# Kernel optimization log

Hardware: AMD Instinct MI355X
Metric: run time of the kernel (lower is better)

Reference implementation:

```python
import jax, jax.numpy as jnp
import numpy as np

N, IN, OUT, RANK = 8192, 4096, 4096, 16
SCALING = 2.0

def setup_inputs() -> dict:
    key = jax.random.key(0)
    k1, k2, k3, k4 = jax.random.split(key, 4)
    x = jax.random.normal(k1, (N, IN), dtype=jnp.float32)
    weight = jax.random.normal(k2, (OUT, IN), dtype=jnp.float32) * (1.0 / np.sqrt(IN))
    lora_A = jax.random.normal(k3, (RANK, IN), dtype=jnp.float32) * (1.0 / np.sqrt(IN))
    lora_B = jax.random.normal(k4, (OUT, RANK), dtype=jnp.float32) * 0.01
    return {"x": x, "weight": weight, "lora_A": lora_A, "lora_B": lora_B}

def reference(x, weight, lora_A, lora_B):
    # frozen base linear: F.linear(x, weight) == x @ weight.T  -> [N, OUT]
    base = jnp.einsum('ni,oi->no', x, weight)
    # LoRA branch: dropout(x) (p=0 => identity) @ A.T @ B.T, scaled
    lora = jnp.einsum('ni,ri->nr', x, lora_A)      # [N, RANK]
    lora = jnp.einsum('nr,or->no', lora, lora_B)   # [N, OUT]
    return base + lora * SCALING
```

## Files before the change

### kernel.cpp

```cpp
#include <hip/hip_runtime.h>


#define N_ROWS 8192
#define K_DIM  4096
#define N_COLS 4096
#define RANK   16
#define BK     64
#define NT     (K_DIM / BK)

#define XBLK ((N_ROWS * K_DIM / 4) / 256)
#define WBLK ((N_COLS * K_DIM / 4) / 256)

typedef __bf16 bf16x8 __attribute__((ext_vector_type(8)));
typedef float  f32x4  __attribute__((ext_vector_type(4)));

__device__ __forceinline__ unsigned short f2bf(float f) {
  unsigned int u = __builtin_bit_cast(unsigned int, f);
  u += 0x7FFFu + ((u >> 16) & 1u);
  return (unsigned short)(u >> 16);
}


__global__ __launch_bounds__(256) void prep_kernel(const float* __restrict__ x,
                                                   const float* __restrict__ w,
                                                   const float* __restrict__ A,
                                                   const float* __restrict__ Bm,
                                                   unsigned short* __restrict__ xb,
                                                   unsigned short* __restrict__ wb) {
  const int b = blockIdx.x;
  if (b < XBLK) {
    size_t idx = (size_t)b * 256 + threadIdx.x;
    const float4 v = *reinterpret_cast<const float4*>(x + idx * 4);
    ushort4 r;
    r.x = f2bf(v.x); r.y = f2bf(v.y); r.z = f2bf(v.z); r.w = f2bf(v.w);
    *reinterpret_cast<ushort4*>(xb + idx * 4) = r;
  } else {
    size_t idx = (size_t)(b - XBLK) * 256 + threadIdx.x;
    int o  = (int)(idx >> 10);
    int ic = (int)(idx & 1023) << 2;
    const float4 wv = *reinterpret_cast<const float4*>(w + (size_t)o * K_DIM + ic);
    float a0 = wv.x, a1 = wv.y, a2 = wv.z, a3 = wv.w;
    float br[RANK];
#pragma unroll
    for (int r4 = 0; r4 < RANK / 4; ++r4) {
      const float4 bv = *reinterpret_cast<const float4*>(Bm + (size_t)o * RANK + r4 * 4);
      br[r4 * 4 + 0] = bv.x; br[r4 * 4 + 1] = bv.y;
      br[r4 * 4 + 2] = bv.z; br[r4 * 4 + 3] = bv.w;
    }
#pragma unroll
    for (int r = 0; r < RANK; ++r) {
      const float4 av = *reinterpret_cast<const float4*>(A + (size_t)r * K_DIM + ic);
      float b2 = br[r] * 2.0f;
      a0 += b2 * av.x; a1 += b2 * av.y; a2 += b2 * av.z; a3 += b2 * av.w;
    }
    ushort4 rr;
    rr.x = f2bf(a0); rr.y = f2bf(a1); rr.z = f2bf(a2); rr.w = f2bf(a3);
    *reinterpret_cast<ushort4*>(wb + (size_t)o * K_DIM + ic) = rr;
  }
}


__device__ __forceinline__ void gload_lds16(const void* g, void* l) {
  __builtin_amdgcn_global_load_lds(
      (__attribute__((address_space(1))) void*)g,
      (__attribute__((address_space(3))) void*)l, 16, 0, 0);
}

__global__ __launch_bounds__(512, 1) void gemm_bf16_r7(
    const unsigned short* __restrict__ xb, const unsigned short* __restrict__ wb,
    float* __restrict__ out) {
  __shared__ __align__(16) char smem[131072];

  const int t  = threadIdx.x;
  const int l  = t & 63;
  const int wv = t >> 6;
  const int lr = l & 15;
  const int lk = l >> 4;
  const int wr = wv >> 2;
  const int wc = wv & 3;

  const int bid  = blockIdx.x;
  const int sbid = (bid & 7) * 64 + (bid >> 3);
  const int bm   = sbid >> 4;
  const int bn   = sbid & 15;

  const int srow = t >> 3;
  const int scol = ((t & 7) ^ ((t >> 3) & 7)) << 3;
  const unsigned short* gA = xb + (size_t)(bm * 256 + srow) * K_DIM + scol;
  const unsigned short* gB = wb + (size_t)(bn * 256 + srow) * K_DIM + scol;
  char* ldsA = smem + t * 16;
  char* ldsB = smem + 65536 + t * 16;

#define STG_A(hh, SRC, NB) do {                                                 \
    const unsigned short* _g = (SRC) + (size_t)((hh) * 128) * K_DIM;            \
    char* _l = ldsA + (NB) + (hh) * 16384;                                      \
    gload_lds16(_g, _l);                                                        \
    gload_lds16(_g + (size_t)64 * K_DIM, _l + 8192);                            \
  } while (0)
#define STG_B(hh, SRC, NB) do {                                                 \
    const unsigned short* _g = (SRC) + (size_t)((hh) * 128) * K_DIM;            \
    char* _l = ldsB + (NB) + (hh) * 16384;                                      \
    gload_lds16(_g, _l);                                                        \
    gload_lds16(_g + (size_t)64 * K_DIM, _l + 8192);                            \
  } while (0)

  const int g0   = (lk ^ (lr & 7)) << 4;
  const int g1   = ((lk + 4) ^ (lr & 7)) << 4;
  const int aoff = (wr * 16 + lr) * 128;
  const int boff = (wc * 16 + lr) * 128;

  bf16x8 aF[8];
  bf16x8 bE[4];
  bf16x8 bO[4];
  f32x4 acc[8][4];
#pragma unroll
  for (int m = 0; m < 8; ++m)
#pragma unroll
    for (int n = 0; n < 4; ++n)
      acc[m][n] = (f32x4){0.f, 0.f, 0.f, 0.f};

#define RD_A(BASE) do {                                                         \
    _Pragma("unroll")                                                           \
    for (int m = 0; m < 4; ++m) {                                               \
      aF[2 * m + 0] = *(const bf16x8*)(smem + (BASE) + m * 4096 + aoff + g0);   \
      aF[2 * m + 1] = *(const bf16x8*)(smem + (BASE) + m * 4096 + aoff + g1);   \
    }                                                                           \
  } while (0)
#define RD_B(DST, BASE) do {                                                    \
    _Pragma("unroll")                                                           \
    for (int n = 0; n < 2; ++n) {                                               \
      DST[2 * n + 0] = *(const bf16x8*)(smem + 65536 + (BASE) + n * 8192 + boff + g0); \
      DST[2 * n + 1] = *(const bf16x8*)(smem + 65536 + (BASE) + n * 8192 + boff + g1); \
    }                                                                           \
  } while (0)

#define MFMA_Q(MB, NB0, BF) do {                                                \
    _Pragma("unroll")                                                           \
    for (int mi = 0; mi < 4; ++mi)                                              \
      _Pragma("unroll")                                                         \
      for (int ni = 0; ni < 2; ++ni)                                            \
        _Pragma("unroll")                                                       \
        for (int kk = 0; kk < 2; ++kk)                                          \
          acc[(MB) + mi][(NB0) + ni] = __builtin_amdgcn_mfma_f32_16x16x32_bf16( \
              aF[mi * 2 + kk], BF[ni * 2 + kk], acc[(MB) + mi][(NB0) + ni], 0, 0, 0); \
  } while (0)

#define PRE_LG() do {                                                           \
    __builtin_amdgcn_sched_barrier(0);                                          \
    __builtin_amdgcn_s_barrier();                                               \
    asm volatile("s_waitcnt lgkmcnt(0)");                                       \
    __builtin_amdgcn_sched_barrier(0);                                          \
    __builtin_amdgcn_s_setprio(1);                                              \
  } while (0)
#define PRE_NOLG() do {                                                         \
    __builtin_amdgcn_sched_barrier(0);                                          \
    __builtin_amdgcn_s_barrier();                                               \
    __builtin_amdgcn_sched_barrier(0);                                          \
    __builtin_amdgcn_s_setprio(1);                                              \
  } while (0)
#define POST() do {                                                             \
    __builtin_amdgcn_s_setprio(0);                                              \
    __builtin_amdgcn_sched_barrier(0);                                          \
    __builtin_amdgcn_s_barrier();                                               \
    __builtin_amdgcn_sched_barrier(0);                                          \
  } while (0)
#define POST_VM4() do {                                                         \
    __builtin_amdgcn_s_setprio(0);                                              \
    __builtin_amdgcn_sched_barrier(0);                                          \
    asm volatile("s_waitcnt vmcnt(4)");                                         \
    __builtin_amdgcn_s_barrier();                                               \
    __builtin_amdgcn_sched_barrier(0);                                          \
  } while (0)

#define TILE(CB, NB, T) do {                                                    \
    const int _t1 = ((T) + 1 < NT) ? (T) + 1 : NT - 1;                          \
    const int _t2 = ((T) + 2 < NT) ? (T) + 2 : NT - 1;                          \
    const unsigned short* _sA1 = gA + (size_t)_t1 * BK;                         \
    const unsigned short* _sB1 = gB + (size_t)_t1 * BK;                         \
    const unsigned short* _sA2 = gA + (size_t)_t2 * BK;                         \
    const unsigned short* _sB2 = gB + (size_t)_t2 * BK;                         \
                    \
    STG_A(1, _sA1, NB);                                                         \
    RD_A((CB)); RD_B(bE, (CB));                                                 \
    asm volatile("s_waitcnt lgkmcnt(8)");                                       \
    PRE_LG(); MFMA_Q(0, 0, bE); POST();                                         \
                       \
    STG_B(0, _sB1, NB);                                                         \
    RD_B(bO, (CB) + 16384);                                                     \
    PRE_LG(); MFMA_Q(0, 2, bO); POST();                                         \
                       \
    STG_A(0, _sA2, CB);                                                         \
    RD_A((CB) + 16384);                                                         \
    PRE_LG(); MFMA_Q(4, 2, bO); POST();                                         \
         \
    STG_B(1, _sB2, CB);                                                         \
    PRE_NOLG(); MFMA_Q(4, 0, bE); POST_VM4();                                   \
  } while (0)

  STG_A(0, gA, 0); STG_A(1, gA, 0); STG_B(0, gB, 0); STG_B(1, gB, 0);
  {
    const unsigned short* _pA1 = gA + (size_t)BK;
    const unsigned short* _pB1 = gB + (size_t)BK;
    STG_A(0, _pA1, 32768);
    STG_B(1, _pB1, 32768);
  }
  __builtin_amdgcn_sched_barrier(0);
  asm volatile("s_waitcnt vmcnt(4)");
  __builtin_amdgcn_s_barrier();
  __builtin_amdgcn_sched_barrier(0);

#pragma nounroll
  for (int u = 0; u < NT / 2; ++u) {
    TILE(0, 32768, 2 * u);
    TILE(32768, 0, 2 * u + 1);
  }

  const int orow = bm * 256 + wr * 16 + lk * 4;
  const int ocol = bn * 256 + wc * 16 + lr;
#pragma unroll
  for (int mf = 0; mf < 8; ++mf)
#pragma unroll
    for (int nf = 0; nf < 4; ++nf)
#pragma unroll
      for (int j = 0; j < 4; ++j)
        out[(size_t)(orow + mf * 32 + j) * N_COLS + (ocol + nf * 64)] = acc[mf][nf][j];

#undef STG_A
#undef STG_B
#undef RD_A
#undef RD_B
#undef MFMA_Q
#undef PRE_LG
#undef PRE_NOLG
#undef POST
#undef POST_VM4
#undef TILE
}


__global__ __launch_bounds__(256) void fallback_kernel(const float* __restrict__ x,
                                                       const float* __restrict__ w,
                                                       const float* __restrict__ A,
                                                       const float* __restrict__ Bm,
                                                       float* __restrict__ out) {
  const int o    = blockIdx.x * 256 + threadIdx.x;
  const int nrow = blockIdx.y;
  float bro[RANK];
#pragma unroll
  for (int r = 0; r < RANK; ++r) bro[r] = Bm[(size_t)o * RANK + r] * 2.0f;
  float bacc = 0.f;
  float tacc[RANK];
#pragma unroll
  for (int r = 0; r < RANK; ++r) tacc[r] = 0.f;
  for (int k = 0; k < K_DIM; ++k) {
    float xv = x[(size_t)nrow * K_DIM + k];
    bacc += xv * w[(size_t)o * K_DIM + k];
#pragma unroll
    for (int r = 0; r < RANK; ++r) tacc[r] += xv * A[(size_t)r * K_DIM + k];
  }
  float res = bacc;
#pragma unroll
  for (int r = 0; r < RANK; ++r) res += bro[r] * tacc[r];
  out[(size_t)nrow * N_COLS + o] = res;
}


extern "C" void kernel_launch(void* const* d_in, const int* in_sizes, int n_in,
                              void* d_out, int out_size, void* d_ws, size_t ws_size,
                              hipStream_t stream) {
  const float* x  = (const float*)d_in[0];
  const float* w  = (const float*)d_in[1];
  const float* A  = (const float*)d_in[2];
  const float* Bm = (const float*)d_in[3];
  float* out = (float*)d_out;

  const size_t need = ((size_t)N_ROWS * K_DIM + (size_t)N_COLS * K_DIM) * sizeof(unsigned short);
  if (ws_size < need) {
    dim3 grid(N_COLS / 256, N_ROWS);
    fallback_kernel<<<grid, 256, 0, stream>>>(x, w, A, Bm, out);
    return;
  }

  unsigned short* xb = (unsigned short*)d_ws;
  unsigned short* wb = xb + (size_t)N_ROWS * K_DIM;

  prep_kernel<<<XBLK + WBLK, 256, 0, stream>>>(x, w, A, Bm, xb, wb);

  const int grid_gemm = (N_ROWS / 256) * (N_COLS / 256);
  gemm_bf16_r7<<<grid_gemm, 512, 0, stream>>>(xb, wb, out);
}
```

Baseline: 314.1 us.

## Replace fine-grained interleaved prefetch schedule with simple double-buffered tile loop

Drops the four-phase schedule, which used per-quarter barriers, setprio and a two-tiles-ahead prefetch interleaved with MFMA quarters. Each tile now issues every global->LDS load for the next tile, reads all fragments and runs all MFMAs, then waits for vmcnt(0) and barriers once. This cuts the number of barriers per tile, but global loads only get one tile of compute to hide behind, and the full vmcnt(0) wait can stall. It reads more like a simplification or baseline experiment than a tuned pipeline.

```diff
diff --git a/kernel.cpp b/kernel.cpp
--- a/kernel.cpp
+++ b/kernel.cpp
@@ -66,7 +66,7 @@
       (__attribute__((address_space(3))) void*)l, 16, 0, 0);
 }
 
-__global__ __launch_bounds__(512, 1) void gemm_bf16_r7(
+__global__ __launch_bounds__(512, 1) void gemm_bf16_r8(
     const unsigned short* __restrict__ xb, const unsigned short* __restrict__ wb,
     float* __restrict__ out) {
   __shared__ __align__(16) char smem[131072];
@@ -145,67 +145,34 @@
               aF[mi * 2 + kk], BF[ni * 2 + kk], acc[(MB) + mi][(NB0) + ni], 0, 0, 0); \
   } while (0)
 
-#define PRE_LG() do {                                                           \
+#define TILE(CB, NB, T) do {                                                    \
+    const int _t1 = ((T) + 1 < NT) ? (T) + 1 : NT - 1;                          \
+    const unsigned short* _sA = gA + (size_t)_t1 * BK;                          \
+    const unsigned short* _sB = gB + (size_t)_t1 * BK;                          \
+                                     \
+    STG_A(0, _sA, NB); STG_A(1, _sA, NB);                                       \
+    STG_B(0, _sB, NB); STG_B(1, _sB, NB);                                       \
     __builtin_amdgcn_sched_barrier(0);                                          \
-    __builtin_amdgcn_s_barrier();                                               \
+      \
+    RD_A((CB));                                                                 \
+    RD_B(bE, (CB));                                                             \
+    RD_B(bO, (CB) + 16384);                                                     \
+    MFMA_Q(0, 0, bE);                                                           \
+    MFMA_Q(0, 2, bO);                                                           \
+    RD_A((CB) + 16384);                                                         \
+    MFMA_Q(4, 0, bE);                                                           \
+    MFMA_Q(4, 2, bO);                                                           \
+        \
     asm volatile("s_waitcnt lgkmcnt(0)");                                       \
     __builtin_amdgcn_sched_barrier(0);                                          \
-    __builtin_amdgcn_s_setprio(1);                                              \
-  } while (0)
-#define PRE_NOLG() do {                                                         \
-    __builtin_amdgcn_sched_barrier(0);                                          \
+    asm volatile("s_waitcnt vmcnt(0)");                                         \
     __builtin_amdgcn_s_barrier();                                               \
     __builtin_amdgcn_sched_barrier(0);                                          \
-    __builtin_amdgcn_s_setprio(1);                                              \
-  } while (0)
-#define POST() do {                                                             \
-    __builtin_amdgcn_s_setprio(0);                                              \
-    __builtin_amdgcn_sched_barrier(0);                                          \
-    __builtin_amdgcn_s_barrier();                                               \
-    __builtin_amdgcn_sched_barrier(0);                                          \
-  } while (0)
-#define POST_VM4() do {                                                         \
-    __builtin_amdgcn_s_setprio(0);                                              \
-    __builtin_amdgcn_sched_barrier(0);                                          \
-    asm volatile("s_waitcnt vmcnt(4)");                                         \
-    __builtin_amdgcn_s_barrier();                                               \
-    __builtin_amdgcn_sched_barrier(0);                                          \
-  } while (0)
-
-#define TILE(CB, NB, T) do {                                                    \
-    const int _t1 = ((T) + 1 < NT) ? (T) + 1 : NT - 1;                          \
-    const int _t2 = ((T) + 2 < NT) ? (T) + 2 : NT - 1;                          \
-    const unsigned short* _sA1 = gA + (size_t)_t1 * BK;                         \
-    const unsigned short* _sB1 = gB + (size_t)_t1 * BK;                         \
-    const unsigned short* _sA2 = gA + (size_t)_t2 * BK;                         \
-    const unsigned short* _sB2 = gB + (size_t)_t2 * BK;                         \
-                    \
-    STG_A(1, _sA1, NB);                                                         \
-    RD_A((CB)); RD_B(bE, (CB));                                                 \
-    asm volatile("s_waitcnt lgkmcnt(8)");                                       \
-    PRE_LG(); MFMA_Q(0, 0, bE); POST();                                         \
-                       \
-    STG_B(0, _sB1, NB);                                                         \
-    RD_B(bO, (CB) + 16384);                                                     \
-    PRE_LG(); MFMA_Q(0, 2, bO); POST();                                         \
-                       \
-    STG_A(0, _sA2, CB);                                                         \
-    RD_A((CB) + 16384);                                                         \
-    PRE_LG(); MFMA_Q(4, 2, bO); POST();                                         \
-         \
-    STG_B(1, _sB2, CB);                                                         \
-    PRE_NOLG(); MFMA_Q(4, 0, bE); POST_VM4();                                   \
   } while (0)
 
   STG_A(0, gA, 0); STG_A(1, gA, 0); STG_B(0, gB, 0); STG_B(1, gB, 0);
-  {
-    const unsigned short* _pA1 = gA + (size_t)BK;
-    const unsigned short* _pB1 = gB + (size_t)BK;
-    STG_A(0, _pA1, 32768);
-    STG_B(1, _pB1, 32768);
-  }
   __builtin_amdgcn_sched_barrier(0);
-  asm volatile("s_waitcnt vmcnt(4)");
+  asm volatile("s_waitcnt vmcnt(0)");
   __builtin_amdgcn_s_barrier();
   __builtin_amdgcn_sched_barrier(0);
 
@@ -230,10 +197,6 @@
 #undef RD_A
 #undef RD_B
 #undef MFMA_Q
-#undef PRE_LG
-#undef PRE_NOLG
-#undef POST
-#undef POST_VM4
 #undef TILE
 }
 
@@ -287,5 +250,5 @@
   prep_kernel<<<XBLK + WBLK, 256, 0, stream>>>(x, w, A, Bm, xb, wb);
 
   const int grid_gemm = (N_ROWS / 256) * (N_COLS / 256);
-  gemm_bf16_r7<<<grid_gemm, 512, 0, stream>>>(xb, wb, out);
-}
+  gemm_bf16_r8<<<grid_gemm, 512, 0, stream>>>(xb, wb, out);
+}
```

After: 310.0 us. About the same (-1.3%).

## Switch GEMM inner product to 32x32x16 bf16 MFMA with remapped LDS fragments

Applied to the files above, without the earlier changes.

Replaces the 16x16x32 bf16 MFMA tiling with 32x32x16 MFMA instructions, so each wave computes 4x2 tiles of 32x32 instead of 8x4 tiles of 16x16. LDS fragment reads, the swizzle offsets and the output write-back mapping are reworked to match the new accumulator layout. The aim is fewer MFMA issues and fewer LDS reads per unit of work, since the larger instruction reuses operands more. The output stores now scatter across rows in a different pattern, and the LDS bank-conflict behaviour changes.

```diff
diff --git a/kernel.cpp b/kernel.cpp
--- a/kernel.cpp
+++ b/kernel.cpp
@@ -12,7 +12,7 @@
 #define WBLK ((N_COLS * K_DIM / 4) / 256)
 
 typedef __bf16 bf16x8 __attribute__((ext_vector_type(8)));
-typedef float  f32x4  __attribute__((ext_vector_type(4)));
+typedef float  f32x16 __attribute__((ext_vector_type(16)));
 
 __device__ __forceinline__ unsigned short f2bf(float f) {
   unsigned int u = __builtin_bit_cast(unsigned int, f);
@@ -66,18 +66,18 @@
       (__attribute__((address_space(3))) void*)l, 16, 0, 0);
 }
 
-__global__ __launch_bounds__(512, 1) void gemm_bf16_r7(
+__global__ __launch_bounds__(512, 1) void gemm_bf16_r11(
     const unsigned short* __restrict__ xb, const unsigned short* __restrict__ wb,
     float* __restrict__ out) {
   __shared__ __align__(16) char smem[131072];
 
-  const int t  = threadIdx.x;
-  const int l  = t & 63;
-  const int wv = t >> 6;
-  const int lr = l & 15;
-  const int lk = l >> 4;
-  const int wr = wv >> 2;
-  const int wc = wv & 3;
+  const int t   = threadIdx.x;
+  const int l   = t & 63;
+  const int wv  = t >> 6;
+  const int l31 = l & 31;
+  const int l5  = l >> 5;
+  const int wm  = wv >> 2;
+  const int wn  = wv & 3;
 
   const int bid  = blockIdx.x;
   const int sbid = (bid & 7) * 64 + (bid >> 3);
@@ -104,45 +104,59 @@
     gload_lds16(_g + (size_t)64 * K_DIM, _l + 8192);                            \
   } while (0)
 
-  const int g0   = (lk ^ (lr & 7)) << 4;
-  const int g1   = ((lk + 4) ^ (lr & 7)) << 4;
-  const int aoff = (wr * 16 + lr) * 128;
-  const int boff = (wc * 16 + lr) * 128;
+  const int g0 = ((0 + l5) ^ (l & 7)) << 4;
+  const int g1 = ((2 + l5) ^ (l & 7)) << 4;
+  const int g2 = ((4 + l5) ^ (l & 7)) << 4;
+  const int g3 = ((6 + l5) ^ (l & 7)) << 4;
+  const int base_a = (wm * 32 + l31) * 128;
+  const int base_b = 65536 + (wn * 32 + l31) * 128;
 
   bf16x8 aF[8];
   bf16x8 bE[4];
   bf16x8 bO[4];
-  f32x4 acc[8][4];
-#pragma unroll
-  for (int m = 0; m < 8; ++m)
-#pragma unroll
-    for (int n = 0; n < 4; ++n)
-      acc[m][n] = (f32x4){0.f, 0.f, 0.f, 0.f};
-
-#define RD_A(BASE) do {                                                         \
+  f32x16 acc[4][2];
+#pragma unroll
+  for (int m = 0; m < 4; ++m)
+#pragma unroll
+    for (int n = 0; n < 2; ++n)
+#pragma unroll
+      for (int e = 0; e < 16; ++e)
+        acc[m][n][e] = 0.f;
+
+#define RD_A01(CB_) do {                                                        \
+    aF[0] = *(const bf16x8*)(smem + (CB_) + base_a + g0);                       \
+    aF[1] = *(const bf16x8*)(smem + (CB_) + base_a + g1);                       \
+    aF[2] = *(const bf16x8*)(smem + (CB_) + base_a + g2);                       \
+    aF[3] = *(const bf16x8*)(smem + (CB_) + base_a + g3);                       \
+    aF[4] = *(const bf16x8*)(smem + (CB_) + 8192 + base_a + g0);                \
+    aF[5] = *(const bf16x8*)(smem + (CB_) + 8192 + base_a + g1);                \
+    aF[6] = *(const bf16x8*)(smem + (CB_) + 8192 + base_a + g2);                \
+    aF[7] = *(const bf16x8*)(smem + (CB_) + 8192 + base_a + g3);                \
+  } while (0)
+#define RD_A23(CB_) do {                                                        \
+    aF[0] = *(const bf16x8*)(smem + (CB_) + 16384 + base_a + g0);               \
+    aF[1] = *(const bf16x8*)(smem + (CB_) + 16384 + base_a + g1);               \
+    aF[2] = *(const bf16x8*)(smem + (CB_) + 16384 + base_a + g2);               \
+    aF[3] = *(const bf16x8*)(smem + (CB_) + 16384 + base_a + g3);               \
+    aF[4] = *(const bf16x8*)(smem + (CB_) + 24576 + base_a + g0);               \
+    aF[5] = *(const bf16x8*)(smem + (CB_) + 24576 + base_a + g1);               \
+    aF[6] = *(const bf16x8*)(smem + (CB_) + 24576 + base_a + g2);               \
+    aF[7] = *(const bf16x8*)(smem + (CB_) + 24576 + base_a + g3);               \
+  } while (0)
+#define RD_B(DST, CB_, HOFF) do {                                               \
+    DST[0] = *(const bf16x8*)(smem + (CB_) + (HOFF) + base_b + g0);             \
+    DST[1] = *(const bf16x8*)(smem + (CB_) + (HOFF) + base_b + g1);             \
+    DST[2] = *(const bf16x8*)(smem + (CB_) + (HOFF) + base_b + g2);             \
+    DST[3] = *(const bf16x8*)(smem + (CB_) + (HOFF) + base_b + g3);             \
+  } while (0)
+
+#define MFMA2(M0, NF, BF) do {                                                  \
     _Pragma("unroll")                                                           \
-    for (int m = 0; m < 4; ++m) {                                               \
-      aF[2 * m + 0] = *(const bf16x8*)(smem + (BASE) + m * 4096 + aoff + g0);   \
-      aF[2 * m + 1] = *(const bf16x8*)(smem + (BASE) + m * 4096 + aoff + g1);   \
-    }                                                                           \
-  } while (0)
-#define RD_B(DST, BASE) do {                                                    \
-    _Pragma("unroll")                                                           \
-    for (int n = 0; n < 2; ++n) {                                               \
-      DST[2 * n + 0] = *(const bf16x8*)(smem + 65536 + (BASE) + n * 8192 + boff + g0); \
-      DST[2 * n + 1] = *(const bf16x8*)(smem + 65536 + (BASE) + n * 8192 + boff + g1); \
-    }                                                                           \
-  } while (0)
-
-#define MFMA_Q(MB, NB0, BF) do {                                                \
-    _Pragma("unroll")                                                           \
-    for (int mi = 0; mi < 4; ++mi)                                              \
+    for (int mi = 0; mi < 2; ++mi)                                              \
       _Pragma("unroll")                                                         \
-      for (int ni = 0; ni < 2; ++ni)                                            \
-        _Pragma("unroll")                                                       \
-        for (int kk = 0; kk < 2; ++kk)                                          \
-          acc[(MB) + mi][(NB0) + ni] = __builtin_amdgcn_mfma_f32_16x16x32_bf16( \
-              aF[mi * 2 + kk], BF[ni * 2 + kk], acc[(MB) + mi][(NB0) + ni], 0, 0, 0); \
+      for (int kk = 0; kk < 4; ++kk)                                            \
+        acc[(M0) + mi][(NF)] = __builtin_amdgcn_mfma_f32_32x32x16_bf16(         \
+            aF[mi * 4 + kk], BF[kk], acc[(M0) + mi][(NF)], 0, 0, 0);            \
   } while (0)
 
 #define PRE_LG() do {                                                           \
@@ -179,22 +193,22 @@
     const unsigned short* _sB1 = gB + (size_t)_t1 * BK;                         \
     const unsigned short* _sA2 = gA + (size_t)_t2 * BK;                         \
     const unsigned short* _sB2 = gB + (size_t)_t2 * BK;                         \
-                    \
+               \
     STG_A(1, _sA1, NB);                                                         \
-    RD_A((CB)); RD_B(bE, (CB));                                                 \
+    RD_A01((CB)); RD_B(bE, (CB), 0);                                            \
     asm volatile("s_waitcnt lgkmcnt(8)");                                       \
-    PRE_LG(); MFMA_Q(0, 0, bE); POST();                                         \
-                       \
+    PRE_LG(); MFMA2(0, 0, bE); POST();                                          \
+                         \
     STG_B(0, _sB1, NB);                                                         \
-    RD_B(bO, (CB) + 16384);                                                     \
-    PRE_LG(); MFMA_Q(0, 2, bO); POST();                                         \
+    RD_B(bO, (CB), 16384);                                                      \
+    PRE_LG(); MFMA2(0, 1, bO); POST();                                          \
                        \
     STG_A(0, _sA2, CB);                                                         \
-    RD_A((CB) + 16384);                                                         \
-    PRE_LG(); MFMA_Q(4, 2, bO); POST();                                         \
-         \
+    RD_A23((CB));                                                               \
+    PRE_LG(); MFMA2(2, 1, bO); POST();                                          \
+                \
     STG_B(1, _sB2, CB);                                                         \
-    PRE_NOLG(); MFMA_Q(4, 0, bE); POST_VM4();                                   \
+    PRE_NOLG(); MFMA2(2, 0, bE); POST_VM4();                                    \
   } while (0)
 
   STG_A(0, gA, 0); STG_A(1, gA, 0); STG_B(0, gB, 0); STG_B(1, gB, 0);
@@ -215,21 +229,24 @@
     TILE(32768, 0, 2 * u + 1);
   }
 
-  const int orow = bm * 256 + wr * 16 + lk * 4;
-  const int ocol = bn * 256 + wc * 16 + lr;
-#pragma unroll
-  for (int mf = 0; mf < 8; ++mf)
-#pragma unroll
-    for (int nf = 0; nf < 4; ++nf)
-#pragma unroll
-      for (int j = 0; j < 4; ++j)
-        out[(size_t)(orow + mf * 32 + j) * N_COLS + (ocol + nf * 64)] = acc[mf][nf][j];
+  const int orow = bm * 256 + wm * 32 + l5 * 4;
+  const int ocol = bn * 256 + wn * 32 + l31;
+#pragma unroll
+  for (int mf = 0; mf < 4; ++mf)
+#pragma unroll
+    for (int nf = 0; nf < 2; ++nf)
+#pragma unroll
+      for (int reg = 0; reg < 16; ++reg) {
+        const int row = orow + mf * 64 + (reg & 3) + 8 * (reg >> 2);
+        out[(size_t)row * N_COLS + (ocol + nf * 128)] = acc[mf][nf][reg];
+      }
 
 #undef STG_A
 #undef STG_B
-#undef RD_A
+#undef RD_A01
+#undef RD_A23
 #undef RD_B
-#undef MFMA_Q
+#undef MFMA2
 #undef PRE_LG
 #undef PRE_NOLG
 #undef POST
@@ -287,5 +304,5 @@
   prep_kernel<<<XBLK + WBLK, 256, 0, stream>>>(x, w, A, Bm, xb, wb);
 
   const int grid_gemm = (N_ROWS / 256) * (N_COLS / 256);
-  gemm_bf16_r7<<<grid_gemm, 512, 0, stream>>>(xb, wb, out);
-}
+  gemm_bf16_r11<<<grid_gemm, 512, 0, stream>>>(xb, wb, out);
+}
```

New measurement: 347.8 us. +10.8%, slower.
